# Kernel optimization log

Measured on AMD Instinct MI355X. Metric: run time of the kernel, lower is better.

## Reference

```python
import jax, jax.numpy as jnp
import numpy as np

N, D, E = 100000, 128, 1600000
BN_EPS = 1e-5

def setup_inputs() -> dict:
    key = jax.random.key(0)
    k1, k2, k3 = jax.random.split(key, 3)
    src_embeddings = jax.random.normal(k1, (N, D), dtype=jnp.float32)
    dst_embeddings = jax.random.normal(k2, (N, D), dtype=jnp.float32)
    graph = jax.random.randint(k3, (2, E), 0, N, dtype=jnp.int64)
    bn_weight = jnp.ones((1,), dtype=jnp.float32)
    bn_bias = jnp.zeros((1,), dtype=jnp.float32)
    return {
        "src_embeddings": src_embeddings,
        "dst_embeddings": dst_embeddings,
        "graph": graph,
        "bn_weight": bn_weight,
        "bn_bias": bn_bias,
    }

def reference(src_embeddings, dst_embeddings, graph, bn_weight, bn_bias):
    # gather endpoint embeddings by edge indices: [E, D]
    src = src_embeddings[graph[0]]
    dst = dst_embeddings[graph[1]]
    # squared distance per edge, clamped as in torch .clamp(min=1e-12)
    d2 = jnp.clip(jnp.sum((src - dst) ** 2, axis=-1), 1e-12, None)  # [E]
    likelihood = -jnp.log(d2)
    # BatchNorm1d(1) in training mode: batch mean, biased variance, eps=1e-5
    mu = jnp.mean(likelihood)
    var = jnp.mean((likelihood - mu) ** 2)
    edge_weights_logits = bn_weight[0] * (likelihood - mu) * jax.lax.rsqrt(var + BN_EPS) + bn_bias[0]
    # weighting_function = torch.sigmoid
    edge_weights = jax.nn.sigmoid(edge_weights_logits)
    # normalize=True: divide by mean
    edge_weights = edge_weights / jnp.mean(edge_weights)
    edge_weights = edge_weights[:, None]  # [E, 1]
    return graph, edge_weights, edge_weights_logits
```

## Files before the change

kernel.cpp:

```cpp
#include <hip/hip_runtime.h>
#include <math.h>

#define EMB_D 128
#define BN_EPS 1e-5f
#define CHUNK 6144
#define RUN_TILE 128

#define QSCALE 22.0f
#define INV_QS2 (1.0f / (QSCALE * QSCALE))

typedef float v4f __attribute__((ext_vector_type(4)));
typedef unsigned int v4u __attribute__((ext_vector_type(4)));

#if defined(__has_builtin)
#if __has_builtin(__builtin_amdgcn_sdot4)
#define SDOT4_HW 1
#endif
#endif

__device__ __forceinline__ int sdot4i(unsigned int a, unsigned int b, int c) {
#ifdef SDOT4_HW
    return __builtin_amdgcn_sdot4((int)a, (int)b, c, false);
#else
    int s = c;
    s += (((int)a << 24) >> 24) * (((int)b << 24) >> 24);
    s += (((int)a << 16) >> 24) * (((int)b << 16) >> 24);
    s += (((int)a << 8)  >> 24) * (((int)b << 8)  >> 24);
    s += ((int)a >> 24) * ((int)b >> 24);
    return s;
#endif
}

__device__ __forceinline__ unsigned int q4(float4 v) {
    const int a = (int)rintf(fminf(fmaxf(v.x * QSCALE, -127.0f), 127.0f));
    const int b = (int)rintf(fminf(fmaxf(v.y * QSCALE, -127.0f), 127.0f));
    const int c = (int)rintf(fminf(fmaxf(v.z * QSCALE, -127.0f), 127.0f));
    const int d = (int)rintf(fminf(fmaxf(v.w * QSCALE, -127.0f), 127.0f));
    return (unsigned int)(a & 0xff) | ((unsigned int)(b & 0xff) << 8)
         | ((unsigned int)(c & 0xff) << 16) | ((unsigned int)(d & 0xff) << 24);
}

__device__ __forceinline__ int d2_dword(unsigned int a, unsigned int b, int m) {
    const int pab = sdot4i(a, b, 0);
    m = sdot4i(a, a, m);
    m = sdot4i(b, b, m);
    return m - 2 * pab;
}

__global__ void prep_bin_kernel(const float* __restrict__ src,
                                const float* __restrict__ dst,
                                unsigned int* __restrict__ src8,
                                unsigned int* __restrict__ dst8,
                                long long N,
                                const int* __restrict__ g,
                                long long E,
                                float* __restrict__ out_graph,
                                unsigned int* __restrict__ rec32,
                                unsigned short* __restrict__ boff,
                                unsigned short* __restrict__ inv16,
                                long long nchunks,
                                int slice_sz,
                                float inv_slice)
{
    const long long nthreads = (long long)gridDim.x * blockDim.x;
    const long long tid0 = (long long)blockIdx.x * blockDim.x + threadIdx.x;

    {
        const long long nvec16 = N * 8;
        for (long long i = tid0; i < nvec16; i += nthreads) {
            const float4* p = (const float4*)src + i * 4;
            v4u w;
            w.x = q4(p[0]); w.y = q4(p[1]); w.z = q4(p[2]); w.w = q4(p[3]);
            __builtin_nontemporal_store(w, (v4u*)src8 + i);
        }
        for (long long i = tid0; i < nvec16; i += nthreads) {
            const float4* p = (const float4*)dst + i * 4;
            v4u w;
            w.x = q4(p[0]); w.y = q4(p[1]); w.z = q4(p[2]); w.w = q4(p[3]);
            __builtin_nontemporal_store(w, (v4u*)dst8 + i);
        }
    }

    __shared__ unsigned int hist[64];
    __shared__ unsigned int curs[64];

    for (long long c = blockIdx.x; c < nchunks; c += gridDim.x) {
        const long long base = c * CHUNK;
        const int cnt = (int)((E - base) < CHUNK ? (E - base) : CHUNK);

        if (threadIdx.x < 64) hist[threadIdx.x] = 0;
        __syncthreads();

        for (int t = threadIdx.x; t < cnt; t += blockDim.x) {
            const long long e = base + t;
            const unsigned int s = (unsigned int)g[e];
            const unsigned int d = (unsigned int)g[E + e];
            int bs = (int)((float)s * inv_slice); bs = bs > 7 ? 7 : bs;
            int bd = (int)((float)d * inv_slice); bd = bd > 7 ? 7 : bd;
            atomicAdd(&hist[bs * 8 + bd], 1u);
        }
        __syncthreads();

        if (threadIdx.x < 64) {
            const unsigned int v = hist[threadIdx.x];
            unsigned int inc = v;
            #pragma unroll
            for (int ofs = 1; ofs < 64; ofs <<= 1) {
                const unsigned int o = __shfl_up(inc, ofs, 64);
                if ((int)threadIdx.x >= ofs) inc += o;
            }
            const unsigned int excl = inc - v;
            curs[threadIdx.x] = excl;
            boff[c * 64 + threadIdx.x] = (unsigned short)excl;
        }
        __syncthreads();

        for (int t = threadIdx.x; t < cnt; t += blockDim.x) {
            const long long e = base + t;
            const unsigned int s = (unsigned int)g[e];
            const unsigned int d = (unsigned int)g[E + e];
            __builtin_nontemporal_store((float)s, &out_graph[e]);
            __builtin_nontemporal_store((float)d, &out_graph[E + e]);
            int bs = (int)((float)s * inv_slice); bs = bs > 7 ? 7 : bs;
            int bd = (int)((float)d * inv_slice); bd = bd > 7 ? 7 : bd;
            const int b = bs * 8 + bd;
            const unsigned int pos = atomicAdd(&curs[b], 1u);
            const unsigned int sl = s - (unsigned int)(bs * slice_sz);
            const unsigned int dl = d - (unsigned int)(bd * slice_sz);
            rec32[base + pos] = sl | (dl << 14);
            inv16[e] = (unsigned short)pos;
        }
        __syncthreads();
    }
}

__global__ void edge_l_binned_kernel(const uint4* __restrict__ src8,
                                     const uint4* __restrict__ dst8,
                                     const unsigned int* __restrict__ rec32,
                                     const unsigned short* __restrict__ boff,
                                     long long nchunks,
                                     long long E,
                                     int slice_sz,
                                     float* __restrict__ L_rec,
                                     double* __restrict__ acc)
{
    const int tid = threadIdx.x;
    const int sub = tid & 7;
    const int grp = tid >> 3;
    const int xcd = (int)(blockIdx.x & 7);
    const long long c = (long long)(blockIdx.x >> 3);

    double sumL = 0.0, sumL2 = 0.0;

    if (c < nchunks) {
        const long long base = c * CHUNK;
        const int cnt = (int)((E - base) < CHUNK ? (E - base) : CHUNK);
        const int sBase = xcd * slice_sz;

        for (int j = 0; j < 8; ++j) {
            const int b = xcd * 8 + j;
            const int start = (int)boff[c * 64 + b];
            const int end = (b == 63) ? cnt : (int)boff[c * 64 + b + 1];
            const int len = end - start;
            const long long rbase = base + start;
            const int dBase = j * slice_sz;

            for (int t0 = 0; t0 < len; t0 += RUN_TILE) {
                bool ok[4];
                int tt[4], ss[4], dd[4];
                #pragma unroll
                for (int q = 0; q < 4; ++q) {
                    const int t = t0 + grp + q * 32;
                    ok[q] = t < len;
                    tt[q] = ok[q] ? t : 0;
                    const unsigned int r = rec32[rbase + tt[q]];
                    ss[q] = sBase + (int)(r & 0x3FFFu);
                    dd[q] = dBase + (int)((r >> 14) & 0x3FFFu);
                }

                int mq[4];
                #pragma unroll
                for (int q = 0; q < 4; ++q) {
                    const uint4 A = src8[(long long)ss[q] * 8 + sub];
                    const uint4 B = dst8[(long long)dd[q] * 8 + sub];
                    int m = d2_dword(A.x, B.x, 0);
                    m = d2_dword(A.y, B.y, m);
                    m = d2_dword(A.z, B.z, m);
                    m = d2_dword(A.w, B.w, m);
                    mq[q] = m;
                }
                #pragma unroll
                for (int q = 0; q < 4; ++q) {
                    mq[q] += __shfl_xor(mq[q], 1, 64);
                    mq[q] += __shfl_xor(mq[q], 2, 64);
                    mq[q] += __shfl_xor(mq[q], 4, 64);
                }

                if (sub == 0) {
                    #pragma unroll
                    for (int q = 0; q < 4; ++q) {
                        if (ok[q]) {
                            const float d2 = (float)mq[q] * INV_QS2;
                            const float L = -logf(fmaxf(d2, 1e-12f));
                            L_rec[rbase + tt[q]] = L;
                            sumL  += (double)L;
                            sumL2 += (double)L * (double)L;
                        }
                    }
                }
            }
        }
    }

    __shared__ double sA[256];
    __shared__ double sB[256];
    sA[tid] = sumL;
    sB[tid] = sumL2;
    __syncthreads();
    for (int ofs = 128; ofs >= 1; ofs >>= 1) {
        if (tid < ofs) {
            sA[tid] += sA[tid + ofs];
            sB[tid] += sB[tid + ofs];
        }
        __syncthreads();
    }
    if (tid == 0) {
        atomicAdd(&acc[0], sA[0]);
        atomicAdd(&acc[1], sB[0]);
    }
}

__global__ void sig_z_kernel(float* __restrict__ zrec,
                             long long E,
                             const double* __restrict__ acc,
                             double* __restrict__ sig_acc,
                             const float* __restrict__ bn_w,
                             const float* __restrict__ bn_b)
{
    const long long nthreads = (long long)gridDim.x * blockDim.x;
    const long long tid0 = (long long)blockIdx.x * blockDim.x + threadIdx.x;

    __shared__ float s_mu, s_inv, s_w, s_b;
    if (threadIdx.x == 0) {
        const double mu  = acc[0] / (double)E;
        const double var = acc[1] / (double)E - mu * mu;
        s_mu  = (float)mu;
        s_inv = (float)(1.0 / sqrt(var + (double)BN_EPS));
        s_w   = bn_w[0];
        s_b   = bn_b[0];
    }
    __syncthreads();
    const float mu = s_mu, iv = s_inv, w = s_w, b = s_b;

    double sig = 0.0;
    const long long nvec = E / 4;
    for (long long i = tid0; i < nvec; i += nthreads) {
        float4 L = ((const float4*)zrec)[i];
        float4 z;
        z.x = w * (L.x - mu) * iv + b;
        z.y = w * (L.y - mu) * iv + b;
        z.z = w * (L.z - mu) * iv + b;
        z.w = w * (L.w - mu) * iv + b;
        ((float4*)zrec)[i] = z;
        const float sx = 1.0f / (1.0f + expf(-z.x));
        const float sy = 1.0f / (1.0f + expf(-z.y));
        const float sz = 1.0f / (1.0f + expf(-z.z));
        const float sw2 = 1.0f / (1.0f + expf(-z.w));
        sig += (double)(sx + sy) + (double)(sz + sw2);
    }
    for (long long i = nvec * 4 + tid0; i < E; i += nthreads) {
        const float L = zrec[i];
        const float z = w * (L - mu) * iv + b;
        zrec[i] = z;
        sig += (double)(1.0f / (1.0f + expf(-z)));
    }

    __shared__ double sS[256];
    sS[threadIdx.x] = sig;
    __syncthreads();
    for (int ofs = 128; ofs >= 1; ofs >>= 1) {
        if ((int)threadIdx.x < ofs)
            sS[threadIdx.x] += sS[threadIdx.x + ofs];
        __syncthreads();
    }
    if (threadIdx.x == 0)
        atomicAdd(sig_acc, sS[0]);
}

__global__ void finalize_kernel(const unsigned short* __restrict__ inv16,
                                const float* __restrict__ zrec,
                                float* __restrict__ logits,
                                float* __restrict__ ew,
                                const double* __restrict__ sig_acc,
                                long long E,
                                long long nchunks)
{
    __shared__ float zs[CHUNK];
    const float scale = (float)((double)E / sig_acc[0]);

    for (long long c = blockIdx.x; c < nchunks; c += gridDim.x) {
        const long long base = c * CHUNK;
        const int cnt = (int)((E - base) < CHUNK ? (E - base) : CHUNK);

        __syncthreads();
        for (int t = threadIdx.x; t < cnt; t += blockDim.x)
            zs[t] = zrec[base + t];
        __syncthreads();

        for (int t = threadIdx.x; t < cnt; t += blockDim.x) {
            const long long e = base + t;
            const float z = zs[inv16[e]];
            __builtin_nontemporal_store(z, &logits[e]);
            __builtin_nontemporal_store(scale / (1.0f + expf(-z)), &ew[e]);
        }
    }
}

__global__ void prep_kernel(const float* __restrict__ src,
                            const float* __restrict__ dst,
                            unsigned int* __restrict__ src8,
                            unsigned int* __restrict__ dst8,
                            long long N,
                            const int* __restrict__ g,
                            long long E,
                            float* __restrict__ out_graph)
{
    const long long nthreads = (long long)gridDim.x * blockDim.x;
    const long long tid0 = (long long)blockIdx.x * blockDim.x + threadIdx.x;
    const long long nvec16 = N * 8;

    for (long long i = tid0; i < nvec16; i += nthreads) {
        const float4* p = (const float4*)src + i * 4;
        v4u w;
        w.x = q4(p[0]); w.y = q4(p[1]); w.z = q4(p[2]); w.w = q4(p[3]);
        __builtin_nontemporal_store(w, (v4u*)src8 + i);
    }
    for (long long i = tid0; i < nvec16; i += nthreads) {
        const float4* p = (const float4*)dst + i * 4;
        v4u w;
        w.x = q4(p[0]); w.y = q4(p[1]); w.z = q4(p[2]); w.w = q4(p[3]);
        __builtin_nontemporal_store(w, (v4u*)dst8 + i);
    }

    const long long gvec = (2 * E) / 4;
    for (long long i = tid0; i < gvec; i += nthreads) {
        const int4 v = ((const int4*)g)[i];
        v4f f;
        f.x = (float)v.x; f.y = (float)v.y; f.z = (float)v.z; f.w = (float)v.w;
        __builtin_nontemporal_store(f, (v4f*)out_graph + i);
    }
    for (long long i = gvec * 4 + tid0; i < 2 * E; i += nthreads)
        out_graph[i] = (float)g[i];
}

__global__ void edge_l_i8_kernel(const uint4* __restrict__ src8,
                                 const uint4* __restrict__ dst8,
                                 const int* __restrict__ g,
                                 long long E,
                                 float* __restrict__ l_out,
                                 double* __restrict__ acc)
{
    const int tid = threadIdx.x;
    const int sub = tid & 7;
    const int grp = tid >> 3;
    const long long blkSpan = 64;
    const long long stride = (long long)gridDim.x * blkSpan;

    double sumL = 0.0, sumL2 = 0.0;

    for (long long base = (long long)blockIdx.x * blkSpan; base < E; base += stride) {
        const long long e1 = base + (long long)grp * 2;
        const long long e2 = e1 + 1;
        const bool ok1 = e1 < E;
        const bool ok2 = e2 < E;

        int s1 = 0, d1 = 0, s2 = 0, d2i = 0;
        if (ok1) { s1 = g[e1]; d1 = g[E + e1]; }
        if (ok2) { s2 = g[e2]; d2i = g[E + e2]; }

        const uint4 A1 = src8[(long long)s1 * 8 + sub];
        const uint4 B1 = dst8[(long long)d1 * 8 + sub];
        const uint4 A2 = src8[(long long)s2 * 8 + sub];
        const uint4 B2 = dst8[(long long)d2i * 8 + sub];

        int m1 = d2_dword(A1.x, B1.x, 0);
        m1 = d2_dword(A1.y, B1.y, m1);
        m1 = d2_dword(A1.z, B1.z, m1);
        m1 = d2_dword(A1.w, B1.w, m1);
        int m2 = d2_dword(A2.x, B2.x, 0);
        m2 = d2_dword(A2.y, B2.y, m2);
        m2 = d2_dword(A2.z, B2.z, m2);
        m2 = d2_dword(A2.w, B2.w, m2);

        m1 += __shfl_xor(m1, 1, 64);
        m1 += __shfl_xor(m1, 2, 64);
        m1 += __shfl_xor(m1, 4, 64);
        m2 += __shfl_xor(m2, 1, 64);
        m2 += __shfl_xor(m2, 2, 64);
        m2 += __shfl_xor(m2, 4, 64);

        if (sub == 0) {
            if (ok1) {
                const float L = -logf(fmaxf((float)m1 * INV_QS2, 1e-12f));
                l_out[e1] = L;
                sumL  += (double)L;
                sumL2 += (double)L * (double)L;
            }
            if (ok2) {
                const float L = -logf(fmaxf((float)m2 * INV_QS2, 1e-12f));
                l_out[e2] = L;
                sumL  += (double)L;
                sumL2 += (double)L * (double)L;
            }
        }
    }

    __shared__ double sA[256];
    __shared__ double sB[256];
    sA[tid] = sumL;
    sB[tid] = sumL2;
    __syncthreads();
    for (int ofs = 128; ofs >= 1; ofs >>= 1) {
        if (tid < ofs) {
            sA[tid] += sA[tid + ofs];
            sB[tid] += sB[tid + ofs];
        }
        __syncthreads();
    }
    if (tid == 0) {
        atomicAdd(&acc[0], sA[0]);
        atomicAdd(&acc[1], sB[0]);
    }
}

__global__ void edge_l_kernel(const float* __restrict__ src,
                              const float* __restrict__ dst,
                              const int*   __restrict__ g,
                              long long E,
                              float*  __restrict__ l_out,
                              double* __restrict__ acc)
{
    const int sub  = threadIdx.x & 7;
    const int egrp = threadIdx.x >> 3;
    const long long stride = (long long)gridDim.x * 32;

    double sumL = 0.0, sumL2 = 0.0;

    long long e = (long long)blockIdx.x * 32 + egrp;
    int s = 0, d = 0;
    if (e < E) { s = g[e]; d = g[E + e]; }

    while (e < E) {
        const long long en = e + stride;
        int sn = 0, dn = 0;
        if (en < E) { sn = g[en]; dn = g[E + en]; }

        const float4* sa = (const float4*)(src + (long long)s * EMB_D);
        const float4* sb = (const float4*)(dst + (long long)d * EMB_D);
        const float4 a0 = sa[sub];      const float4 b0 = sb[sub];
        const float4 a1 = sa[sub + 8];  const float4 b1 = sb[sub + 8];
        const float4 a2 = sa[sub + 16]; const float4 b2 = sb[sub + 16];
        const float4 a3 = sa[sub + 24]; const float4 b3 = sb[sub + 24];

        float dx, dy, dz, dw, p = 0.f;
        dx = a0.x-b0.x; dy = a0.y-b0.y; dz = a0.z-b0.z; dw = a0.w-b0.w;
        p += fmaf(dx,dx,fmaf(dy,dy,fmaf(dz,dz,dw*dw)));
        dx = a1.x-b1.x; dy = a1.y-b1.y; dz = a1.z-b1.z; dw = a1.w-b1.w;
        p += fmaf(dx,dx,fmaf(dy,dy,fmaf(dz,dz,dw*dw)));
        dx = a2.x-b2.x; dy = a2.y-b2.y; dz = a2.z-b2.z; dw = a2.w-b2.w;
        p += fmaf(dx,dx,fmaf(dy,dy,fmaf(dz,dz,dw*dw)));
        dx = a3.x-b3.x; dy = a3.y-b3.y; dz = a3.z-b3.z; dw = a3.w-b3.w;
        p += fmaf(dx,dx,fmaf(dy,dy,fmaf(dz,dz,dw*dw)));

        p += __shfl_xor(p, 1, 64);
        p += __shfl_xor(p, 2, 64);
        p += __shfl_xor(p, 4, 64);

        if (sub == 0) {
            const float L = -logf(fmaxf(p, 1e-12f));
            l_out[e] = L;
            sumL  += (double)L;
            sumL2 += (double)L * (double)L;
        }
        e = en; s = sn; d = dn;
    }

    __shared__ double sA[256];
    __shared__ double sB[256];
    sA[threadIdx.x] = sumL;
    sB[threadIdx.x] = sumL2;
    __syncthreads();
    for (int ofs = 128; ofs >= 1; ofs >>= 1) {
        if ((int)threadIdx.x < ofs) {
            sA[threadIdx.x] += sA[threadIdx.x + ofs];
            sB[threadIdx.x] += sB[threadIdx.x + ofs];
        }
        __syncthreads();
    }
    if (threadIdx.x == 0) {
        atomicAdd(&acc[0], sA[0]);
        atomicAdd(&acc[1], sB[0]);
    }
}

__global__ void graph_copy_kernel(const int* __restrict__ g,
                                  float* __restrict__ out_graph,
                                  long long E2)
{
    const long long nth = (long long)gridDim.x * blockDim.x;
    for (long long i = (long long)blockIdx.x * blockDim.x + threadIdx.x;
         i < E2; i += nth)
        out_graph[i] = (float)g[i];
}

__global__ void bn_sig_kernel(float* __restrict__ logits,
                              const double* __restrict__ acc,
                              double* __restrict__ sig_acc,
                              const float* __restrict__ bn_w,
                              const float* __restrict__ bn_b,
                              long long E)
{
    const long long nthreads = (long long)gridDim.x * blockDim.x;
    const long long tid0 = (long long)blockIdx.x * blockDim.x + threadIdx.x;

    __shared__ float s_mu, s_inv, s_w, s_b;
    if (threadIdx.x == 0) {
        const double mu  = acc[0] / (double)E;
        const double var = acc[1] / (double)E - mu * mu;
        s_mu  = (float)mu;
        s_inv = (float)(1.0 / sqrt(var + (double)BN_EPS));
        s_w   = bn_w[0];
        s_b   = bn_b[0];
    }
    __syncthreads();
    const float mu = s_mu, inv = s_inv, w = s_w, b = s_b;

    double sig = 0.0;
    const long long nvec = E / 4;
    for (long long i = tid0; i < nvec; i += nthreads) {
        float4 L = ((const float4*)logits)[i];
        float4 z;
        z.x = w * (L.x - mu) * inv + b;
        z.y = w * (L.y - mu) * inv + b;
        z.z = w * (L.z - mu) * inv + b;
        z.w = w * (L.w - mu) * inv + b;
        ((float4*)logits)[i] = z;
        const float sx = 1.0f / (1.0f + expf(-z.x));
        const float sy = 1.0f / (1.0f + expf(-z.y));
        const float sz = 1.0f / (1.0f + expf(-z.z));
        const float sw2 = 1.0f / (1.0f + expf(-z.w));
        sig += (double)(sx + sy) + (double)(sz + sw2);
    }
    for (long long i = nvec * 4 + tid0; i < E; i += nthreads) {
        const float L = logits[i];
        const float z = w * (L - mu) * inv + b;
        logits[i] = z;
        sig += (double)(1.0f / (1.0f + expf(-z)));
    }

    __shared__ double sS[256];
    sS[threadIdx.x] = sig;
    __syncthreads();
    for (int ofs = 128; ofs >= 1; ofs >>= 1) {
        if ((int)threadIdx.x < ofs)
            sS[threadIdx.x] += sS[threadIdx.x + ofs];
        __syncthreads();
    }
    if (threadIdx.x == 0)
        atomicAdd(sig_acc, sS[0]);
}

__global__ void norm_kernel(const float* __restrict__ logits,
                            float* __restrict__ ew,
                            const double* __restrict__ sig_acc,
                            long long E)
{
    const long long nthreads = (long long)gridDim.x * blockDim.x;
    const long long tid0 = (long long)blockIdx.x * blockDim.x + threadIdx.x;
    const float scale = (float)((double)E / sig_acc[0]);

    const long long nvec = E / 4;
    for (long long i = tid0; i < nvec; i += nthreads) {
        const float4 z = ((const float4*)logits)[i];
        v4f v;
        v.x = scale / (1.0f + expf(-z.x));
        v.y = scale / (1.0f + expf(-z.y));
        v.z = scale / (1.0f + expf(-z.z));
        v.w = scale / (1.0f + expf(-z.w));
        __builtin_nontemporal_store(v, (v4f*)ew + i);
    }
    for (long long i = nvec * 4 + tid0; i < E; i += nthreads)
        ew[i] = scale / (1.0f + expf(-logits[i]));
}

extern "C" void kernel_launch(void* const* d_in, const int* in_sizes, int n_in,
                              void* d_out, int out_size, void* d_ws, size_t ws_size,
                              hipStream_t stream) {
    const float* src  = (const float*)d_in[0];
    const float* dst  = (const float*)d_in[1];
    const int*   g    = (const int*)d_in[2];
    const float* bn_w = (const float*)d_in[3];
    const float* bn_b = (const float*)d_in[4];

    const long long N = (long long)in_sizes[0] / EMB_D;
    const long long E = (long long)in_sizes[2] / 2;

    float* out        = (float*)d_out;
    float* out_graph  = out;
    float* out_ew     = out + 2 * E;
    float* out_logits = out + 3 * E;

    const long long nchunks = (E + CHUNK - 1) / CHUNK;
    const long long SLOTS = nchunks * CHUNK;

    double*       acc  = (double*)d_ws;
    unsigned char* src8 = (unsigned char*)d_ws + 512;
    unsigned char* dst8 = src8 + (size_t)N * EMB_D;
    unsigned int* rec32 = (unsigned int*)(dst8 + (size_t)N * EMB_D);
    float* L_rec = (float*)(rec32 + SLOTS);
    unsigned short* inv16 = (unsigned short*)(L_rec + SLOTS);
    unsigned short* boff  = inv16 + SLOTS;

    const size_t need_t3 = 512 + (size_t)N * EMB_D * 2;
    const size_t need_t1 = need_t3 + (size_t)SLOTS * 10 + (size_t)nchunks * 128;

    const int slice_sz = (int)((N + 7) / 8);
    const float inv_slice = 1.0f / (float)slice_sz;
    const bool pack_ok = (slice_sz < 16384) && (E < (1LL << 31));

    (void)hipMemsetAsync(d_ws, 0, 512, stream);

    if (ws_size >= need_t1 && pack_ok) {
        prep_bin_kernel<<<4096, 256, 0, stream>>>(src, dst,
                                                  (unsigned int*)src8,
                                                  (unsigned int*)dst8,
                                                  N, g, E, out_graph,
                                                  rec32, boff, inv16,
                                                  nchunks, slice_sz, inv_slice);
        edge_l_binned_kernel<<<(unsigned int)(8 * nchunks), 256, 0, stream>>>(
            (const uint4*)src8, (const uint4*)dst8, rec32, boff,
            nchunks, E, slice_sz, L_rec, acc);
        sig_z_kernel<<<1024, 256, 0, stream>>>(L_rec, E, acc, &acc[2],
                                               bn_w, bn_b);
        finalize_kernel<<<(unsigned int)nchunks, 256, 0, stream>>>(
            inv16, L_rec, out_logits, out_ew, &acc[2], E, nchunks);
    } else if (ws_size >= need_t3) {
        prep_kernel<<<4096, 256, 0, stream>>>(src, dst,
                                              (unsigned int*)src8,
                                              (unsigned int*)dst8,
                                              N, g, E, out_graph);
        edge_l_i8_kernel<<<4096, 256, 0, stream>>>((const uint4*)src8,
                                                   (const uint4*)dst8,
                                                   g, E, out_logits, acc);
        bn_sig_kernel<<<1024, 256, 0, stream>>>(out_logits, acc, &acc[2],
                                                bn_w, bn_b, E);
        norm_kernel<<<1024, 256, 0, stream>>>(out_logits, out_ew, &acc[2], E);
    } else {
        edge_l_kernel<<<4096, 256, 0, stream>>>(src, dst, g, E, out_logits, acc);
        bn_sig_kernel<<<1024, 256, 0, stream>>>(out_logits, acc, &acc[2],
                                                bn_w, bn_b, E);
        norm_kernel<<<1024, 256, 0, stream>>>(out_logits, out_ew, &acc[2], E);
        graph_copy_kernel<<<1024, 256, 0, stream>>>(g, out_graph, 2 * E);
    }
}
```

Measured before the change: 280.6 us.

## Persist binned edge kernel, drop memset, recompute logits in finalize, simplify quantize

Several changes land together. The binned edge kernel now runs on a fixed grid of 2048 blocks that loop over chunks with the bin index as the outer loop, which is meant to improve slice locality in the per-XCD cache. The accumulator memset is replaced by zeroing inside the prep kernel, and the sigmoid-sum kernel no longer writes z back; finalize recomputes z from L instead, saving one full write pass. The quantization loop also changes to one float4 per thread with plain stores in place of nontemporal 16-byte stores, which may change write efficiency.

```diff
diff --git a/kernel.cpp b/kernel.cpp
--- a/kernel.cpp
+++ b/kernel.cpp
@@ -10,7 +10,6 @@
 #define INV_QS2 (1.0f / (QSCALE * QSCALE))
 
 typedef float v4f __attribute__((ext_vector_type(4)));
-typedef unsigned int v4u __attribute__((ext_vector_type(4)));
 
 #if defined(__has_builtin)
 #if __has_builtin(__builtin_amdgcn_sdot4)
@@ -60,25 +59,22 @@
                                 unsigned short* __restrict__ inv16,
                                 long long nchunks,
                                 int slice_sz,
-                                float inv_slice)
-{
+                                float inv_slice,
+                                double* __restrict__ acc)
+{
+    if (blockIdx.x == 0 && threadIdx.x == 0) {
+        acc[0] = 0.0; acc[1] = 0.0; acc[2] = 0.0; acc[3] = 0.0;
+    }
+
     const long long nthreads = (long long)gridDim.x * blockDim.x;
     const long long tid0 = (long long)blockIdx.x * blockDim.x + threadIdx.x;
 
     {
-        const long long nvec16 = N * 8;
-        for (long long i = tid0; i < nvec16; i += nthreads) {
-            const float4* p = (const float4*)src + i * 4;
-            v4u w;
-            w.x = q4(p[0]); w.y = q4(p[1]); w.z = q4(p[2]); w.w = q4(p[3]);
-            __builtin_nontemporal_store(w, (v4u*)src8 + i);
-        }
-        for (long long i = tid0; i < nvec16; i += nthreads) {
-            const float4* p = (const float4*)dst + i * 4;
-            v4u w;
-            w.x = q4(p[0]); w.y = q4(p[1]); w.z = q4(p[2]); w.w = q4(p[3]);
-            __builtin_nontemporal_store(w, (v4u*)dst8 + i);
-        }
+        const long long nvec = N * 32;
+        for (long long i = tid0; i < nvec; i += nthreads)
+            src8[i] = q4(((const float4*)src)[i]);
+        for (long long i = tid0; i < nvec; i += nthreads)
+            dst8[i] = q4(((const float4*)dst)[i]);
     }
 
     __shared__ unsigned int hist[64];
@@ -148,22 +144,23 @@
     const int sub = tid & 7;
     const int grp = tid >> 3;
     const int xcd = (int)(blockIdx.x & 7);
-    const long long c = (long long)(blockIdx.x >> 3);
+    const unsigned int bloc = blockIdx.x >> 3;
+    const unsigned int B = gridDim.x >> 3;
+    const int sBase = xcd * slice_sz;
 
     double sumL = 0.0, sumL2 = 0.0;
 
-    if (c < nchunks) {
-        const long long base = c * CHUNK;
-        const int cnt = (int)((E - base) < CHUNK ? (E - base) : CHUNK);
-        const int sBase = xcd * slice_sz;
-
-        for (int j = 0; j < 8; ++j) {
-            const int b = xcd * 8 + j;
+    for (int j = 0; j < 8; ++j) {
+        const int b = xcd * 8 + j;
+        const int dBase = j * slice_sz;
+
+        for (long long c = bloc; c < nchunks; c += B) {
+            const long long base = c * CHUNK;
+            const int cnt = (int)((E - base) < CHUNK ? (E - base) : CHUNK);
             const int start = (int)boff[c * 64 + b];
             const int end = (b == 63) ? cnt : (int)boff[c * 64 + b + 1];
             const int len = end - start;
             const long long rbase = base + start;
-            const int dBase = j * slice_sz;
 
             for (int t0 = 0; t0 < len; t0 += RUN_TILE) {
                 bool ok[4];
@@ -182,11 +179,11 @@
                 #pragma unroll
                 for (int q = 0; q < 4; ++q) {
                     const uint4 A = src8[(long long)ss[q] * 8 + sub];
-                    const uint4 B = dst8[(long long)dd[q] * 8 + sub];
-                    int m = d2_dword(A.x, B.x, 0);
-                    m = d2_dword(A.y, B.y, m);
-                    m = d2_dword(A.z, B.z, m);
-                    m = d2_dword(A.w, B.w, m);
+                    const uint4 Bv = dst8[(long long)dd[q] * 8 + sub];
+                    int m = d2_dword(A.x, Bv.x, 0);
+                    m = d2_dword(A.y, Bv.y, m);
+                    m = d2_dword(A.z, Bv.z, m);
+                    m = d2_dword(A.w, Bv.w, m);
                     mq[q] = m;
                 }
                 #pragma unroll
@@ -230,12 +227,12 @@
     }
 }
 
-__global__ void sig_z_kernel(float* __restrict__ zrec,
-                             long long E,
-                             const double* __restrict__ acc,
-                             double* __restrict__ sig_acc,
-                             const float* __restrict__ bn_w,
-                             const float* __restrict__ bn_b)
+__global__ void sig_sum_kernel(const float* __restrict__ L_rec,
+                               long long E,
+                               const double* __restrict__ acc,
+                               double* __restrict__ sig_acc,
+                               const float* __restrict__ bn_w,
+                               const float* __restrict__ bn_b)
 {
     const long long nthreads = (long long)gridDim.x * blockDim.x;
     const long long tid0 = (long long)blockIdx.x * blockDim.x + threadIdx.x;
@@ -255,23 +252,19 @@
     double sig = 0.0;
     const long long nvec = E / 4;
     for (long long i = tid0; i < nvec; i += nthreads) {
-        float4 L = ((const float4*)zrec)[i];
-        float4 z;
-        z.x = w * (L.x - mu) * iv + b;
-        z.y = w * (L.y - mu) * iv + b;
-        z.z = w * (L.z - mu) * iv + b;
-        z.w = w * (L.w - mu) * iv + b;
-        ((float4*)zrec)[i] = z;
-        const float sx = 1.0f / (1.0f + expf(-z.x));
-        const float sy = 1.0f / (1.0f + expf(-z.y));
-        const float sz = 1.0f / (1.0f + expf(-z.z));
-        const float sw2 = 1.0f / (1.0f + expf(-z.w));
+        const float4 L = ((const float4*)L_rec)[i];
+        const float z0 = w * (L.x - mu) * iv + b;
+        const float z1 = w * (L.y - mu) * iv + b;
+        const float z2 = w * (L.z - mu) * iv + b;
+        const float z3 = w * (L.w - mu) * iv + b;
+        const float sx = 1.0f / (1.0f + expf(-z0));
+        const float sy = 1.0f / (1.0f + expf(-z1));
+        const float sz = 1.0f / (1.0f + expf(-z2));
+        const float sw2 = 1.0f / (1.0f + expf(-z3));
         sig += (double)(sx + sy) + (double)(sz + sw2);
     }
     for (long long i = nvec * 4 + tid0; i < E; i += nthreads) {
-        const float L = zrec[i];
-        const float z = w * (L - mu) * iv + b;
-        zrec[i] = z;
+        const float z = w * (L_rec[i] - mu) * iv + b;
         sig += (double)(1.0f / (1.0f + expf(-z)));
     }
 
@@ -288,15 +281,29 @@
 }
 
 __global__ void finalize_kernel(const unsigned short* __restrict__ inv16,
-                                const float* __restrict__ zrec,
+                                const float* __restrict__ L_rec,
                                 float* __restrict__ logits,
                                 float* __restrict__ ew,
+                                const double* __restrict__ acc,
                                 const double* __restrict__ sig_acc,
+                                const float* __restrict__ bn_w,
+                                const float* __restrict__ bn_b,
                                 long long E,
                                 long long nchunks)
 {
-    __shared__ float zs[CHUNK];
-    const float scale = (float)((double)E / sig_acc[0]);
+    __shared__ float Ls[CHUNK];
+    __shared__ float s_mu, s_inv, s_w, s_b, s_scale;
+    if (threadIdx.x == 0) {
+        const double mu  = acc[0] / (double)E;
+        const double var = acc[1] / (double)E - mu * mu;
+        s_mu  = (float)mu;
+        s_inv = (float)(1.0 / sqrt(var + (double)BN_EPS));
+        s_w   = bn_w[0];
+        s_b   = bn_b[0];
+        s_scale = (float)((double)E / sig_acc[0]);
+    }
+    __syncthreads();
+    const float mu = s_mu, iv = s_inv, w = s_w, b = s_b, scale = s_scale;
 
     for (long long c = blockIdx.x; c < nchunks; c += gridDim.x) {
         const long long base = c * CHUNK;
@@ -304,12 +311,12 @@
 
         __syncthreads();
         for (int t = threadIdx.x; t < cnt; t += blockDim.x)
-            zs[t] = zrec[base + t];
+            Ls[t] = L_rec[base + t];
         __syncthreads();
 
         for (int t = threadIdx.x; t < cnt; t += blockDim.x) {
             const long long e = base + t;
-            const float z = zs[inv16[e]];
+            const float z = w * (Ls[inv16[e]] - mu) * iv + b;
             __builtin_nontemporal_store(z, &logits[e]);
             __builtin_nontemporal_store(scale / (1.0f + expf(-z)), &ew[e]);
         }
@@ -327,20 +334,12 @@
 {
     const long long nthreads = (long long)gridDim.x * blockDim.x;
     const long long tid0 = (long long)blockIdx.x * blockDim.x + threadIdx.x;
-    const long long nvec16 = N * 8;
-
-    for (long long i = tid0; i < nvec16; i += nthreads) {
-        const float4* p = (const float4*)src + i * 4;
-        v4u w;
-        w.x = q4(p[0]); w.y = q4(p[1]); w.z = q4(p[2]); w.w = q4(p[3]);
-        __builtin_nontemporal_store(w, (v4u*)src8 + i);
-    }
-    for (long long i = tid0; i < nvec16; i += nthreads) {
-        const float4* p = (const float4*)dst + i * 4;
-        v4u w;
-        w.x = q4(p[0]); w.y = q4(p[1]); w.z = q4(p[2]); w.w = q4(p[3]);
-        __builtin_nontemporal_store(w, (v4u*)dst8 + i);
-    }
+    const long long nvec = N * 32;
+
+    for (long long i = tid0; i < nvec; i += nthreads)
+        src8[i] = q4(((const float4*)src)[i]);
+    for (long long i = tid0; i < nvec; i += nthreads)
+        dst8[i] = q4(((const float4*)dst)[i]);
 
     const long long gvec = (2 * E) / 4;
     for (long long i = tid0; i < gvec; i += nthreads) {
@@ -628,23 +627,24 @@
     const float inv_slice = 1.0f / (float)slice_sz;
     const bool pack_ok = (slice_sz < 16384) && (E < (1LL << 31));
 
-    (void)hipMemsetAsync(d_ws, 0, 512, stream);
-
     if (ws_size >= need_t1 && pack_ok) {
         prep_bin_kernel<<<4096, 256, 0, stream>>>(src, dst,
                                                   (unsigned int*)src8,
                                                   (unsigned int*)dst8,
                                                   N, g, E, out_graph,
                                                   rec32, boff, inv16,
-                                                  nchunks, slice_sz, inv_slice);
-        edge_l_binned_kernel<<<(unsigned int)(8 * nchunks), 256, 0, stream>>>(
+                                                  nchunks, slice_sz, inv_slice,
+                                                  acc);
+        edge_l_binned_kernel<<<2048, 256, 0, stream>>>(
             (const uint4*)src8, (const uint4*)dst8, rec32, boff,
             nchunks, E, slice_sz, L_rec, acc);
-        sig_z_kernel<<<1024, 256, 0, stream>>>(L_rec, E, acc, &acc[2],
-                                               bn_w, bn_b);
+        sig_sum_kernel<<<1024, 256, 0, stream>>>(L_rec, E, acc, &acc[2],
+                                                 bn_w, bn_b);
         finalize_kernel<<<(unsigned int)nchunks, 256, 0, stream>>>(
-            inv16, L_rec, out_logits, out_ew, &acc[2], E, nchunks);
+            inv16, L_rec, out_logits, out_ew, acc, &acc[2],
+            bn_w, bn_b, E, nchunks);
     } else if (ws_size >= need_t3) {
+        (void)hipMemsetAsync(d_ws, 0, 512, stream);
         prep_kernel<<<4096, 256, 0, stream>>>(src, dst,
                                               (unsigned int*)src8,
                                               (unsigned int*)dst8,
@@ -656,6 +656,7 @@
                                                 bn_w, bn_b, E);
         norm_kernel<<<1024, 256, 0, stream>>>(out_logits, out_ew, &acc[2], E);
     } else {
+        (void)hipMemsetAsync(d_ws, 0, 512, stream);
         edge_l_kernel<<<4096, 256, 0, stream>>>(src, dst, g, E, out_logits, acc);
         bn_sig_kernel<<<1024, 256, 0, stream>>>(out_logits, acc, &acc[2],
                                                 bn_w, bn_b, E);
```

Measured after the change: 270.9 us. 1.04x faster.
